# Optimization experiments

Hardware: AMD Instinct MI355X
Metric: run time of the kernel (lower is better)

Reference implementation:

```python
import jax, jax.numpy as jnp
import numpy as np

N_LEVELS = 128.0  # int8: [-128, 127]

def fake_quant(x):
    """Per-tensor int8 fixed-point fake quant (power-of-two scale), STE rounding."""
    maxabs = jnp.max(jnp.abs(x))
    # power-of-two scale covering maxabs, as in Brevitas *FixedPoint quantizers
    scale = jnp.exp2(jnp.ceil(jnp.log2(jnp.maximum(maxabs, 1e-10)))) / N_LEVELS
    scale = jax.lax.stop_gradient(scale)
    xs = x / scale
    q = jnp.clip(jnp.round(xs), -N_LEVELS, N_LEVELS - 1.0)
    q = xs + jax.lax.stop_gradient(q - xs)  # straight-through estimator
    return q * scale


def setup_inputs() -> dict:
    key = jax.random.key(0)
    k1, k2, k3, k4 = jax.random.split(key, 4)
    B, T, D, H = 512, 2048, 10, 20
    x = jax.random.normal(k1, (B, T, D), dtype=jnp.float32)
    h0 = jnp.zeros((B, H), dtype=jnp.float32)
    W_ih = jax.random.normal(k2, (H, D), dtype=jnp.float32) * 0.3
    W_hh = jax.random.normal(k3, (H, H), dtype=jnp.float32) * 0.2
    b = jax.random.normal(k4, (H,), dtype=jnp.float32) * 0.1
    return {"x": x, "h0": h0, "W_ih": W_ih, "W_hh": W_hh, "b": b}


def reference(x, h0, W_ih, W_hh, b):
    # io quant on input and initial state
    xq = fake_quant(x)
    h = fake_quant(h0)
    # weight / bias quant (per-tensor fixed point)
    Wi = fake_quant(W_ih)
    Wh = fake_quant(W_hh)
    bq = fake_quant(b)
    # precompute input-hidden contribution for all timesteps: [B,T,H]
    xW = jnp.einsum('btd,hd->bth', xq, Wi) + bq

    def step(h_prev, xw_t):
        acc = xw_t + h_prev @ Wh.T          # gate accumulation [B,H]
        acc = fake_quant(acc)               # gate_acc_quant
        h_new = jnp.tanh(acc)               # vanilla RNN nonlinearity
        out = fake_quant(h_new)             # io_quant on output/hidden
        return out, out

    xW_t = jnp.swapaxes(xW, 0, 1)           # [T,B,H]
    _, outs = jax.lax.scan(step, h, xW_t)   # outs: [T,B,H]
    return jnp.swapaxes(outs, 0, 1)         # batch_first output [B,T,H]
```

## Files before the change

### kernel.cpp

```cpp
#include <hip/hip_runtime.h>
#include <math.h>

#define BB 512
#define TT 2048
#define DD 10
#define HH 20
#define BH (BB*HH)

#define WS_AMAX     0
#define WS_PROD_XWI 4
#define WS_INV_SX   5
#define WS_S_H0     6
#define WS_INV_SH0  7
#define WS_S_WH     8
#define WS_BQ       16
#define WS_WIP      40
#define WS_WHP      104
#define WS_XW_OFF   4096

__device__ __forceinline__ int dot4(int a, int b, int c) {
#if defined(__has_builtin)
#if __has_builtin(__builtin_amdgcn_sdot4)
    return __builtin_amdgcn_sdot4(a, b, c, false);
#define DOT4_DONE 1
#endif
#endif
#ifndef DOT4_DONE
    int r = c;
    r += ((a << 24) >> 24) * ((b << 24) >> 24);
    r += ((a << 16) >> 24) * ((b << 16) >> 24);
    r += ((a << 8) >> 24) * ((b << 8) >> 24);
    r += (a >> 24) * (b >> 24);
    return r;
#endif
}

__device__ __forceinline__ float pow2scale(float m, float* inv) {
    m = fmaxf(m, 1e-10f);
    int e; float f = frexpf(m, &e);
    int k = (f == 0.5f) ? (e - 1) : e;
    *inv = ldexpf(1.f, 7 - k);
    return ldexpf(1.f, k - 7);
}

__device__ __forceinline__ int qlevel(float v, float inv) {
    return (int)fminf(fmaxf(rintf(v * inv), -128.f), 127.f);
}

__device__ __forceinline__ int pack4(int a, int b, int c, int d) {
    return (a & 255) | ((b & 255) << 8) | ((c & 255) << 16) | ((d & 255) << 24);
}

__global__ void k_amax(const float* __restrict__ x, int n4, unsigned* amax) {
    int g = blockIdx.x * blockDim.x + threadIdx.x;
    int stride = gridDim.x * blockDim.x;
    const float4* xv = (const float4*)x;
    float m = 0.f;
    for (int i = g; i < n4; i += stride) {
        float4 v = xv[i];
        m = fmaxf(m, fmaxf(fmaxf(fabsf(v.x), fabsf(v.y)), fmaxf(fabsf(v.z), fabsf(v.w))));
    }
#pragma unroll
    for (int off = 32; off; off >>= 1) m = fmaxf(m, __shfl_xor(m, off, 64));
    if ((threadIdx.x & 63) == 0) atomicMax(amax, __float_as_uint(m));
}

__device__ float bmaxabs(const float* p, int n, float* red, int tid) {
    float m = 0.f;
    for (int i = tid; i < n; i += 256) m = fmaxf(m, fabsf(p[i]));
    red[tid] = m; __syncthreads();
    for (int s = 128; s; s >>= 1) {
        if (tid < s) red[tid] = fmaxf(red[tid], red[tid + s]);
        __syncthreads();
    }
    m = red[0]; __syncthreads();
    return m;
}

__global__ void k_prep(const float* __restrict__ Wi, const float* __restrict__ Wh,
                       const float* __restrict__ bias, const float* __restrict__ h0,
                       float* wsf, int* wsi) {
    __shared__ float red[256];
    __shared__ float hdr[4];
    int tid = threadIdx.x;
    float mwi = bmaxabs(Wi, HH * DD, red, tid);
    float mwh = bmaxabs(Wh, HH * HH, red, tid);
    float mb  = bmaxabs(bias, HH, red, tid);
    float mh0 = bmaxabs(h0, BH, red, tid);
    if (tid == 0) {
        float mx = __uint_as_float(((unsigned*)wsf)[WS_AMAX]);
        float isx, iswi, iswh, isb, ish0;
        float sx  = pow2scale(mx,  &isx);
        float swi = pow2scale(mwi, &iswi);
        float swh = pow2scale(mwh, &iswh);
        float sb  = pow2scale(mb,  &isb);
        float sh0 = pow2scale(mh0, &ish0);
        wsf[WS_PROD_XWI] = sx * swi;
        wsf[WS_INV_SX]   = isx;
        wsf[WS_S_H0]     = sh0;
        wsf[WS_INV_SH0]  = ish0;
        wsf[WS_S_WH]     = swh;
        hdr[0] = iswi; hdr[1] = iswh; hdr[2] = sb; hdr[3] = isb;
    }
    __syncthreads();
    if (tid < HH) {
        float iswi = hdr[0], iswh = hdr[1], sb = hdr[2], isb = hdr[3];
        int lv[20];
#pragma unroll
        for (int d = 0; d < DD; ++d) lv[d] = qlevel(Wi[tid * DD + d], iswi);
        lv[10] = 0; lv[11] = 0;
#pragma unroll
        for (int k = 0; k < 3; ++k)
            wsi[WS_WIP + tid * 3 + k] = pack4(lv[4*k], lv[4*k+1], lv[4*k+2], lv[4*k+3]);
#pragma unroll
        for (int k = 0; k < HH; ++k) lv[k] = qlevel(Wh[tid * HH + k], iswh);
#pragma unroll
        for (int k = 0; k < 5; ++k)
            wsi[WS_WHP + tid * 5 + k] = pack4(lv[4*k], lv[4*k+1], lv[4*k+2], lv[4*k+3]);
        wsf[WS_BQ + tid] = (float)qlevel(bias[tid], isb) * sb;
    }
}

__global__ __launch_bounds__(256) void k_xw(const float* __restrict__ x,
                                            const float* __restrict__ wsf,
                                            const int* __restrict__ wsi,
                                            float* __restrict__ xw) {
    int g = blockIdx.x * 256 + threadIdx.x;
    int t = g & (TT - 1);
    int b = g >> 11;
    float isx  = wsf[WS_INV_SX];
    float prod = wsf[WS_PROD_XWI];
    const float2* xp = (const float2*)(x + (size_t)g * DD);
    float xv[10];
#pragma unroll
    for (int k = 0; k < 5; ++k) { float2 v = xp[k]; xv[2*k] = v.x; xv[2*k+1] = v.y; }
    int lv[12];
#pragma unroll
    for (int d = 0; d < DD; ++d) lv[d] = qlevel(xv[d], isx);
    lv[10] = 0; lv[11] = 0;
    int xpk[3];
#pragma unroll
    for (int k = 0; k < 3; ++k) xpk[k] = pack4(lv[4*k], lv[4*k+1], lv[4*k+2], lv[4*k+3]);
    float res[20];
#pragma unroll
    for (int j = 0; j < HH; ++j) {
        int ai = 0;
#pragma unroll
        for (int k = 0; k < 3; ++k) ai = dot4(xpk[k], wsi[WS_WIP + j * 3 + k], ai);
        res[j] = (float)ai * prod + wsf[WS_BQ + j];
    }
    float4* op = (float4*)(xw + (size_t)t * BH + b * HH);
#pragma unroll
    for (int k = 0; k < 5; ++k)
        op[k] = make_float4(res[4*k], res[4*k+1], res[4*k+2], res[4*k+3]);
}

__global__ __launch_bounds__(1024) void k_rnn(const float* __restrict__ h0,
                                              const float* __restrict__ wsf,
                                              const int* __restrict__ wsi,
                                              float* __restrict__ xw) {
    __shared__ signed char hq[BH];
    __shared__ float wred[32];
    __shared__ float bc[8];
    __shared__ int lut[256];
    const int tid = threadIdx.x;
    const int b = tid >> 1;
    const int jb = (tid & 1) * 10;
    const float s_wh = wsf[WS_S_WH];
    float sprod = wsf[WS_S_H0] * s_wh;

    int whp[50];
#pragma unroll
    for (int jj = 0; jj < 10; ++jj)
#pragma unroll
        for (int k = 0; k < 5; ++k)
            whp[jj * 5 + k] = wsi[WS_WHP + (jb + jj) * 5 + k];

    {
        float ish0 = wsf[WS_INV_SH0];
        const float* hp = h0 + b * HH + jb;
        int lv[10];
#pragma unroll
        for (int i = 0; i < 10; ++i) lv[i] = qlevel(hp[i], ish0);
#pragma unroll
        for (int k = 0; k < 5; ++k)
            *(short*)&hq[b * HH + jb + 2 * k] = (short)((lv[2*k] & 255) | ((lv[2*k+1] & 255) << 8));
    }
    float xwA[10];
    {
        const float2* p = (const float2*)(xw + b * HH + jb);
#pragma unroll
        for (int k = 0; k < 5; ++k) { float2 v = p[k]; xwA[2*k] = v.x; xwA[2*k+1] = v.y; }
    }
    __syncthreads();

    for (int t = 0; t < TT; ++t) {
        float xwB[10];
        if (t + 1 < TT) {
            const float2* p = (const float2*)(xw + (size_t)(t + 1) * BH + b * HH + jb);
#pragma unroll
            for (int k = 0; k < 5; ++k) { float2 v = p[k]; xwB[2*k] = v.x; xwB[2*k+1] = v.y; }
        }
        int hd[5];
        const int* hrow = (const int*)(hq + b * HH);
#pragma unroll
        for (int k = 0; k < 5; ++k) hd[k] = hrow[k];
        float acc[10];
#pragma unroll
        for (int jj = 0; jj < 10; ++jj) {
            int ai = 0;
#pragma unroll
            for (int k = 0; k < 5; ++k) ai = dot4(hd[k], whp[jj * 5 + k], ai);
            acc[jj] = xwA[jj] + (float)ai * sprod;
        }
        float mx = acc[0], mn = acc[0];
#pragma unroll
        for (int jj = 1; jj < 10; ++jj) { mx = fmaxf(mx, acc[jj]); mn = fminf(mn, acc[jj]); }
#pragma unroll
        for (int off = 32; off; off >>= 1) {
            mx = fmaxf(mx, __shfl_xor(mx, off, 64));
            mn = fminf(mn, __shfl_xor(mn, off, 64));
        }
        if ((tid & 63) == 0) { wred[tid >> 6] = mx; wred[16 + (tid >> 6)] = mn; }
        __syncthreads();
        if (tid == 0) {
            float ma = wred[0], mi = wred[16];
#pragma unroll
            for (int w = 1; w < 16; ++w) { ma = fmaxf(ma, wred[w]); mi = fminf(mi, wred[16 + w]); }
            float isa; float sa = pow2scale(fmaxf(ma, -mi), &isa);
            float lp = fminf(fmaxf(rintf(ma * isa), -128.f), 127.f);
            float ln = fminf(fmaxf(rintf(mi * isa), -128.f), 127.f);
            float mlvl = fmaxf(fabsf(lp), fabsf(ln));
            float mh = tanhf(mlvl * sa);
            float ish; float sh = pow2scale(mh, &ish);
            bc[0] = sa; bc[1] = isa; bc[2] = sh; bc[3] = ish; bc[4] = sh * s_wh;
        }
        __syncthreads();
        float sa = bc[0], isa = bc[1], sh = bc[2], ish = bc[3];
        sprod = bc[4];
        if (tid < 256) {
            float tq = tanhf((float)(tid - 128) * sa);
            lut[tid] = (int)fminf(fmaxf(rintf(tq * ish), -128.f), 127.f);
        }
        __syncthreads();
        int ql[10];
#pragma unroll
        for (int jj = 0; jj < 10; ++jj) {
            int li = (int)fminf(fmaxf(rintf(acc[jj] * isa), -128.f), 127.f) + 128;
            ql[jj] = lut[li];
        }
        {
            float2* op = (float2*)(xw + (size_t)t * BH + b * HH + jb);
#pragma unroll
            for (int k = 0; k < 5; ++k) {
                float2 v; v.x = (float)ql[2*k] * sh; v.y = (float)ql[2*k+1] * sh;
                op[k] = v;
            }
        }
#pragma unroll
        for (int k = 0; k < 5; ++k)
            *(short*)&hq[b * HH + jb + 2 * k] = (short)((ql[2*k] & 255) | ((ql[2*k+1] & 255) << 8));
#pragma unroll
        for (int jj = 0; jj < 10; ++jj) xwA[jj] = xwB[jj];
        __syncthreads();
    }
}

__global__ __launch_bounds__(256) void k_tr(const float* __restrict__ src, float* __restrict__ out) {
    __shared__ float tile[16 * 16 * HH];
    int t0 = blockIdx.x * 16, b0 = blockIdx.y * 16;
    for (int i = threadIdx.x; i < 16 * 16 * HH; i += 256) {
        int r = i / (16 * HH), c = i % (16 * HH);
        tile[i] = src[(size_t)(t0 + r) * BH + b0 * HH + c];
    }
    __syncthreads();
    for (int i = threadIdx.x; i < 16 * 16 * HH; i += 256) {
        int bb = i / (16 * HH), rj = i % (16 * HH);
        int r = rj / HH, j = rj % HH;
        out[(size_t)(b0 + bb) * (TT * HH) + (t0 + r) * HH + j] = tile[r * (16 * HH) + bb * HH + j];
    }
}

extern "C" void kernel_launch(void* const* d_in, const int* in_sizes, int n_in,
                              void* d_out, int out_size, void* d_ws, size_t ws_size,
                              hipStream_t stream) {
    const float* x    = (const float*)d_in[0];
    const float* h0   = (const float*)d_in[1];
    const float* Wi   = (const float*)d_in[2];
    const float* Wh   = (const float*)d_in[3];
    const float* bias = (const float*)d_in[4];
    float* out = (float*)d_out;

    char* w = (char*)d_ws;
    float* wsf = (float*)w;
    int* wsi = (int*)w;
    unsigned* amax = (unsigned*)w;
    float* xw = (float*)(w + WS_XW_OFF);

    hipMemsetAsync(d_ws, 0, 64, stream);
    int n = in_sizes[0];
    k_amax<<<2048, 256, 0, stream>>>(x, n / 4, amax);
    k_prep<<<1, 256, 0, stream>>>(Wi, Wh, bias, h0, wsf, wsi);
    k_xw<<<(BB * TT) / 256, 256, 0, stream>>>(x, wsf, wsi, xw);
    k_rnn<<<1, 1024, 0, stream>>>(h0, wsf, wsi, xw);
    k_tr<<<dim3(TT / 16, BB / 16), 256, 0, stream>>>(xw, out);
}
```

Measured before the change: 5.611 ms.

## Exchange hidden state via lane shuffles and cut per-step barriers in RNN kernel

The recurrent kernel now keeps the quantized hidden row in registers and exchanges halves between paired lanes with shuffles, instead of going through shared memory. This removes one of the four block barriers per timestep. The serial tid==0 reduction is replaced by a parallel wave-level reduction in the first 256 threads, which also build the LUT in the same phase, and the remaining barriers use a custom lgkmcnt wait plus s_barrier. The power-of-two scale now comes from bit manipulation instead of frexp/ldexp, and k_xw is reindexed so its output writes are coalesced over batch. The trade-off is that correctness now depends on the hand-written barrier and the shuffle packing being right.

Result: faster. 5.369 ms (-4.3%).

```diff
diff --git a/kernel.cpp b/kernel.cpp
--- a/kernel.cpp
+++ b/kernel.cpp
@@ -17,6 +17,8 @@
 #define WS_WIP      40
 #define WS_WHP      104
 #define WS_XW_OFF   4096
+
+#define BAR() asm volatile("s_waitcnt lgkmcnt(0)\n\ts_barrier" ::: "memory")
 
 __device__ __forceinline__ int dot4(int a, int b, int c) {
 #if defined(__has_builtin)
@@ -35,12 +37,12 @@
 #endif
 }
 
-__device__ __forceinline__ float pow2scale(float m, float* inv) {
+__device__ __forceinline__ void p2s(float m, float* s, float* is) {
     m = fmaxf(m, 1e-10f);
-    int e; float f = frexpf(m, &e);
-    int k = (f == 0.5f) ? (e - 1) : e;
-    *inv = ldexpf(1.f, 7 - k);
-    return ldexpf(1.f, k - 7);
+    unsigned u = __float_as_uint(m);
+    int k = (int)(u >> 23) - 127 + ((u & 0x7fffffu) ? 1 : 0);
+    *s  = __uint_as_float((unsigned)(k + 120) << 23);
+    *is = __uint_as_float((unsigned)(134 - k) << 23);
 }
 
 __device__ __forceinline__ int qlevel(float v, float inv) {
@@ -89,12 +91,12 @@
     float mh0 = bmaxabs(h0, BH, red, tid);
     if (tid == 0) {
         float mx = __uint_as_float(((unsigned*)wsf)[WS_AMAX]);
-        float isx, iswi, iswh, isb, ish0;
-        float sx  = pow2scale(mx,  &isx);
-        float swi = pow2scale(mwi, &iswi);
-        float swh = pow2scale(mwh, &iswh);
-        float sb  = pow2scale(mb,  &isb);
-        float sh0 = pow2scale(mh0, &ish0);
+        float sx, isx, swi, iswi, swh, iswh, sb, isb, sh0, ish0;
+        p2s(mx,  &sx,  &isx);
+        p2s(mwi, &swi, &iswi);
+        p2s(mwh, &swh, &iswh);
+        p2s(mb,  &sb,  &isb);
+        p2s(mh0, &sh0, &ish0);
         wsf[WS_PROD_XWI] = sx * swi;
         wsf[WS_INV_SX]   = isx;
         wsf[WS_S_H0]     = sh0;
@@ -126,11 +128,11 @@
                                             const int* __restrict__ wsi,
                                             float* __restrict__ xw) {
     int g = blockIdx.x * 256 + threadIdx.x;
-    int t = g & (TT - 1);
-    int b = g >> 11;
+    int b = g & (BB - 1);
+    int t = g >> 9;
     float isx  = wsf[WS_INV_SX];
     float prod = wsf[WS_PROD_XWI];
-    const float2* xp = (const float2*)(x + (size_t)g * DD);
+    const float2* xp = (const float2*)(x + ((size_t)b * TT + t) * DD);
     float xv[10];
 #pragma unroll
     for (int k = 0; k < 5; ++k) { float2 v = xp[k]; xv[2*k] = v.x; xv[2*k+1] = v.y; }
@@ -159,13 +161,13 @@
                                               const float* __restrict__ wsf,
                                               const int* __restrict__ wsi,
                                               float* __restrict__ xw) {
-    __shared__ signed char hq[BH];
-    __shared__ float wred[32];
-    __shared__ float bc[8];
+    __shared__ float2 wred[16];
+    __shared__ float4 bc;
     __shared__ int lut[256];
     const int tid = threadIdx.x;
     const int b = tid >> 1;
     const int jb = (tid & 1) * 10;
+    const bool isLo = (tid & 1) == 0;
     const float s_wh = wsf[WS_S_WH];
     float sprod = wsf[WS_S_H0] * s_wh;
 
@@ -176,15 +178,29 @@
         for (int k = 0; k < 5; ++k)
             whp[jj * 5 + k] = wsi[WS_WHP + (jb + jj) * 5 + k];
 
+    int hd[5];
     {
         float ish0 = wsf[WS_INV_SH0];
-        const float* hp = h0 + b * HH + jb;
+        const float2* hp = (const float2*)(h0 + b * HH + jb);
         int lv[10];
 #pragma unroll
-        for (int i = 0; i < 10; ++i) lv[i] = qlevel(hp[i], ish0);
-#pragma unroll
-        for (int k = 0; k < 5; ++k)
-            *(short*)&hq[b * HH + jb + 2 * k] = (short)((lv[2*k] & 255) | ((lv[2*k+1] & 255) << 8));
+        for (int k = 0; k < 5; ++k) {
+            float2 v = hp[k];
+            lv[2*k]   = qlevel(v.x, ish0);
+            lv[2*k+1] = qlevel(v.y, ish0);
+        }
+        int PA = pack4(lv[0], lv[1], lv[2], lv[3]);
+        int PB = pack4(lv[4], lv[5], lv[6], lv[7]);
+        int PC = (lv[8] & 255) | ((lv[9] & 255) << 8);
+        int QA = __shfl_xor(PA, 1, 64);
+        int QB = __shfl_xor(PB, 1, 64);
+        int QC = __shfl_xor(PC, 1, 64);
+        int XA = isLo ? PA : QA, XB = isLo ? PB : QB, XC = isLo ? PC : QC;
+        int YA = isLo ? QA : PA, YB = isLo ? QB : PB, YC = isLo ? QC : PC;
+        hd[0] = XA; hd[1] = XB;
+        hd[2] = (XC & 0xFFFF) | (YA << 16);
+        hd[3] = ((unsigned)YA >> 16) | (YB << 16);
+        hd[4] = ((unsigned)YB >> 16) | (YC << 16);
     }
     float xwA[10];
     {
@@ -192,7 +208,6 @@
 #pragma unroll
         for (int k = 0; k < 5; ++k) { float2 v = p[k]; xwA[2*k] = v.x; xwA[2*k+1] = v.y; }
     }
-    __syncthreads();
 
     for (int t = 0; t < TT; ++t) {
         float xwB[10];
@@ -201,10 +216,6 @@
 #pragma unroll
             for (int k = 0; k < 5; ++k) { float2 v = p[k]; xwB[2*k] = v.x; xwB[2*k+1] = v.y; }
         }
-        int hd[5];
-        const int* hrow = (const int*)(hq + b * HH);
-#pragma unroll
-        for (int k = 0; k < 5; ++k) hd[k] = hrow[k];
         float acc[10];
 #pragma unroll
         for (int jj = 0; jj < 10; ++jj) {
@@ -213,56 +224,74 @@
             for (int k = 0; k < 5; ++k) ai = dot4(hd[k], whp[jj * 5 + k], ai);
             acc[jj] = xwA[jj] + (float)ai * sprod;
         }
-        float mx = acc[0], mn = acc[0];
-#pragma unroll
-        for (int jj = 1; jj < 10; ++jj) { mx = fmaxf(mx, acc[jj]); mn = fminf(mn, acc[jj]); }
+        float mx = acc[0], nmi = -acc[0];
+#pragma unroll
+        for (int jj = 1; jj < 10; ++jj) { mx = fmaxf(mx, acc[jj]); nmi = fmaxf(nmi, -acc[jj]); }
 #pragma unroll
         for (int off = 32; off; off >>= 1) {
-            mx = fmaxf(mx, __shfl_xor(mx, off, 64));
-            mn = fminf(mn, __shfl_xor(mn, off, 64));
-        }
-        if ((tid & 63) == 0) { wred[tid >> 6] = mx; wred[16 + (tid >> 6)] = mn; }
-        __syncthreads();
-        if (tid == 0) {
-            float ma = wred[0], mi = wred[16];
-#pragma unroll
-            for (int w = 1; w < 16; ++w) { ma = fmaxf(ma, wred[w]); mi = fminf(mi, wred[16 + w]); }
-            float isa; float sa = pow2scale(fmaxf(ma, -mi), &isa);
+            mx  = fmaxf(mx,  __shfl_xor(mx,  off, 64));
+            nmi = fmaxf(nmi, __shfl_xor(nmi, off, 64));
+        }
+        if ((tid & 63) == 0) wred[tid >> 6] = make_float2(mx, nmi);
+        BAR();
+        float isa, sh;
+        float sprodN;
+        if (tid < 256) {
+            float2 p = wred[tid & 15];
+            float ma = p.x, nm = p.y;
+#pragma unroll
+            for (int off = 8; off; off >>= 1) {
+                ma = fmaxf(ma, __shfl_xor(ma, off, 64));
+                nm = fmaxf(nm, __shfl_xor(nm, off, 64));
+            }
+            float sa;
+            p2s(fmaxf(ma, nm), &sa, &isa);
             float lp = fminf(fmaxf(rintf(ma * isa), -128.f), 127.f);
-            float ln = fminf(fmaxf(rintf(mi * isa), -128.f), 127.f);
+            float ln = fminf(fmaxf(rintf(-nm * isa), -128.f), 127.f);
             float mlvl = fmaxf(fabsf(lp), fabsf(ln));
             float mh = tanhf(mlvl * sa);
-            float ish; float sh = pow2scale(mh, &ish);
-            bc[0] = sa; bc[1] = isa; bc[2] = sh; bc[3] = ish; bc[4] = sh * s_wh;
-        }
-        __syncthreads();
-        float sa = bc[0], isa = bc[1], sh = bc[2], ish = bc[3];
-        sprod = bc[4];
-        if (tid < 256) {
+            float ish;
+            p2s(mh, &sh, &ish);
+            sprodN = sh * s_wh;
             float tq = tanhf((float)(tid - 128) * sa);
             lut[tid] = (int)fminf(fmaxf(rintf(tq * ish), -128.f), 127.f);
-        }
-        __syncthreads();
+            if (tid == 0) bc = make_float4(isa, sh, sprodN, 0.f);
+        }
+        BAR();
+        if (tid >= 256) {
+            float4 v = bc;
+            isa = v.x; sh = v.y; sprod = v.z;
+        } else {
+            sprod = sprodN;
+        }
         int ql[10];
 #pragma unroll
         for (int jj = 0; jj < 10; ++jj) {
-            int li = (int)fminf(fmaxf(rintf(acc[jj] * isa), -128.f), 127.f) + 128;
-            ql[jj] = lut[li];
+            int qi = (int)fminf(fmaxf(rintf(acc[jj] * isa), -128.f), 127.f);
+            ql[jj] = lut[128 + qi];
         }
         {
             float2* op = (float2*)(xw + (size_t)t * BH + b * HH + jb);
 #pragma unroll
-            for (int k = 0; k < 5; ++k) {
-                float2 v; v.x = (float)ql[2*k] * sh; v.y = (float)ql[2*k+1] * sh;
-                op[k] = v;
-            }
-        }
-#pragma unroll
-        for (int k = 0; k < 5; ++k)
-            *(short*)&hq[b * HH + jb + 2 * k] = (short)((ql[2*k] & 255) | ((ql[2*k+1] & 255) << 8));
+            for (int k = 0; k < 5; ++k)
+                op[k] = make_float2((float)ql[2*k] * sh, (float)ql[2*k+1] * sh);
+        }
+        {
+            int PA = pack4(ql[0], ql[1], ql[2], ql[3]);
+            int PB = pack4(ql[4], ql[5], ql[6], ql[7]);
+            int PC = (ql[8] & 255) | ((ql[9] & 255) << 8);
+            int QA = __shfl_xor(PA, 1, 64);
+            int QB = __shfl_xor(PB, 1, 64);
+            int QC = __shfl_xor(PC, 1, 64);
+            int XA = isLo ? PA : QA, XB = isLo ? PB : QB, XC = isLo ? PC : QC;
+            int YA = isLo ? QA : PA, YB = isLo ? QB : PB, YC = isLo ? QC : PC;
+            hd[0] = XA; hd[1] = XB;
+            hd[2] = (XC & 0xFFFF) | (YA << 16);
+            hd[3] = ((unsigned)YA >> 16) | (YB << 16);
+            hd[4] = ((unsigned)YB >> 16) | (YC << 16);
+        }
 #pragma unroll
         for (int jj = 0; jj < 10; ++jj) xwA[jj] = xwB[jj];
-        __syncthreads();
     }
 }
 
```
